# Kernel optimization log

Hardware: AMD Instinct MI355X
Metric: run time of the kernel (lower is better)

The kernel has to match this reference:

```python
import jax, jax.numpy as jnp
import numpy as np

WS, OWS, HEADS, DH = 8, 12, 4, 16
INNER = HEADS * DH
DIM = 64
RATIO = 0.5
REL = 12  # rel_size = WS + (OWS - WS)


def _conv1x1(x, W, b):
    return jnp.einsum('oc,bchw->bohw', W, x) + b[None, :, None, None]


def _lrelu(x):
    return jnp.where(x >= 0, x, 0.1 * x)


def _rel_to_abs(x):
    # x: [b, l, 2r-1] -> [b, l, r]
    b, l, m = x.shape
    r = (m + 1) // 2
    x = jnp.pad(x, ((0, 0), (0, 0), (0, 1))).reshape(b, l * (m + 1))
    x = jnp.pad(x, ((0, 0), (0, m - l))).reshape(b, l + 1, m)
    return x[:, :l, -r:]


def _relative_logits_1d(q, rel_k):
    # q: [b, h, w, d], rel_k: [2r-1, d] -> [b, h, r, w, r]
    b, h, w, _ = q.shape
    r = (rel_k.shape[0] + 1) // 2
    logits = jnp.einsum('bxyd,rd->bxyr', q, rel_k)
    logits = _rel_to_abs(logits.reshape(b * h, w, 2 * r - 1)).reshape(b, h, w, r)
    return jnp.broadcast_to(logits[:, :, None], (b, h, r, w, r))


def _rel_pos_emb(q, rel_h, rel_w):
    # q: [b, WS*WS, DH] -> [b, WS*WS, REL*REL]
    b = q.shape[0]
    q = q.reshape(b, WS, WS, DH)
    lw = _relative_logits_1d(q, rel_w)                        # [b, x, i, y, j]
    lw = lw.transpose(0, 1, 3, 2, 4).reshape(b, WS * WS, REL * REL)   # (x y),(i j)
    lh = _relative_logits_1d(q.transpose(0, 2, 1, 3), rel_h)  # [b, y, i, x, j]
    lh = lh.transpose(0, 3, 1, 4, 2).reshape(b, WS * WS, REL * REL)   # (x y),(j i)
    return lw + lh


def _windows(t, B, Hw, Ww):
    # 'b c (h p1) (w p2) -> b (h w) (p1 p2 c)'
    return t.reshape(B, INNER, Hw, WS, Ww, WS).transpose(0, 2, 4, 3, 5, 1).reshape(B, Hw * Ww, WS * WS * INNER)


def _forward(x, condition_global, Wq, bq, Wk, bk, Wv, bv, Wout, bout,
             rel_h, rel_w, pin_W, pin_b, ln_w, ln_b, sa_W, sa_b,
             m1_W, m1_b, m2_W, m2_b):
    B, C, H, W = x.shape
    Hw, Ww = H // WS, W // WS
    Nw = Hw * Ww
    keep = int(Nw * RATIO)  # deterministic num_keep_node (expected r=0.5)
    scale = DH ** -0.5

    qs = _conv1x1(x, Wq, bq)
    ks = _conv1x1(x, Wk, bk)
    vs = _conv1x1(x, Wv, bv)

    # condition_wind: stacked ij meshgrid of linspace(-1,1,WS), tiled over windows
    lin = jnp.linspace(-1.0, 1.0, WS)
    gy, gx = jnp.meshgrid(lin, lin, indexing='ij')
    wind = jnp.tile(jnp.stack([gy, gx]).astype(x.dtype)[None], (B, 1, Hw, Ww))
    cond = jnp.concatenate([vs, condition_global, wind], axis=1)  # [B, INNER+4, H, W]

    # PredictorLG
    h1 = _conv1x1(cond, pin_W, pin_b)
    u = h1.mean(1, keepdims=True)
    s = ((h1 - u) ** 2).mean(1, keepdims=True)
    h1 = ln_w[None, :, None, None] * (h1 - u) / jnp.sqrt(s + 1e-6) + ln_b[None, :, None, None]
    h1 = _lrelu(h1)
    sa = jax.lax.conv_general_dilated(h1, sa_W, (1, 1), ((1, 1), (1, 1)),
                                      dimension_numbers=('NCHW', 'OIHW', 'NCHW'))
    sa = jax.nn.sigmoid(sa + sa_b[None, :, None, None])          # [B,1,H,W]

    xm = h1.mean(1)                                               # [B,H,W]
    xm = xm.reshape(B, Hw, WS, Ww, WS).transpose(0, 1, 3, 2, 4).reshape(B, Nw, WS * WS)
    z = _lrelu(xm @ m1_W.T + m1_b)
    pred = jax.nn.softmax(z @ m2_W.T + m2_b, axis=-1)
    score = pred[:, :, 0]
    idx = jnp.argsort(-score, axis=1)
    idx1, idx2 = idx[:, :keep], idx[:, keep:]
    bar = jnp.arange(B)[:, None]

    v_easy = vs * sa

    qw = _windows(qs, B, Hw, Ww)                                  # [B, Nw, 64*INNER]

    pad = (OWS - WS) // 2
    def unfold(t):
        p = jax.lax.conv_general_dilated_patches(t, (OWS, OWS), (WS, WS),
                                                 [(pad, pad), (pad, pad)])
        # [B, INNER*OWS*OWS, Hw, Ww], channel-major (c, kh, kw) like torch unfold
        p = p.reshape(B, INNER, OWS * OWS, Nw)
        return p.transpose(0, 3, 2, 1).reshape(B, Nw, OWS * OWS * INNER)  # (j c)
    kw, vw = unfold(ks), unfold(vs)

    qk, kk, vk = qw[bar, idx1], kw[bar, idx1], vw[bar, idx1]       # gather hard windows

    def heads(t, ntok):
        return t.reshape(B * keep, ntok, HEADS, DH).transpose(0, 2, 1, 3).reshape(B * keep * HEADS, ntok, DH)
    qh = heads(qk, WS * WS) * scale
    kh = heads(kk, OWS * OWS)
    vh = heads(vk, OWS * OWS)

    attn = jnp.einsum('bqc,bkc->bqk', qh, kh) + _rel_pos_emb(qh, rel_h, rel_w)
    attn = jax.nn.softmax(attn, axis=-1)
    vo = jnp.einsum('bqk,bkc->bqc', attn, vh)                      # [B*keep*HEADS, 64, DH]

    # '(b j head) (p1 p2) c -> b j (p1 p2 head c)'
    v1 = vo.reshape(B, keep, HEADS, WS * WS, DH).transpose(0, 1, 3, 2, 4).reshape(B, keep, WS * WS * INNER)
    v2 = _windows(v_easy, B, Hw, Ww)[bar, idx2]

    out = jnp.zeros((B, Nw, WS * WS * INNER), x.dtype)
    out = out.at[bar, idx1].set(v1).at[bar, idx2].set(v2)          # batch_index_fill
    # 'b (h w) (dh dw c) -> b c (h dh) (w dw)'
    out = out.reshape(B, Hw, Ww, WS, WS, INNER).transpose(0, 5, 1, 3, 2, 4).reshape(B, INNER, H, W)
    return _conv1x1(out, Wout, bout)


def setup_inputs() -> dict:
    key = jax.random.key(0)
    k = jax.random.split(key, 16)
    B, H, W = 2, 256, 256
    cdim = INNER + 4
    rel_scale = DH ** -0.5

    def p(kk, shape, s=0.05):
        return jax.random.normal(kk, shape, jnp.float32) * s

    return {
        'x': jax.random.normal(k[0], (B, DIM, H, W), jnp.float32),
        'condition_global': jax.random.normal(k[1], (B, 2, H, W), jnp.float32),
        'Wq': p(k[2], (INNER, DIM)), 'bq': jnp.zeros((INNER,), jnp.float32),
        'Wk': p(k[3], (INNER, DIM)), 'bk': jnp.zeros((INNER,), jnp.float32),
        'Wv': p(k[4], (INNER, DIM)), 'bv': jnp.zeros((INNER,), jnp.float32),
        'Wout': p(k[5], (DIM, INNER)), 'bout': jnp.zeros((DIM,), jnp.float32),
        'rel_h': jax.random.normal(k[6], (2 * REL - 1, DH), jnp.float32) * rel_scale,
        'rel_w': jax.random.normal(k[7], (2 * REL - 1, DH), jnp.float32) * rel_scale,
        'pin_W': p(k[8], (cdim // 4, cdim)), 'pin_b': jnp.zeros((cdim // 4,), jnp.float32),
        'ln_w': jnp.ones((cdim // 4,), jnp.float32), 'ln_b': jnp.zeros((cdim // 4,), jnp.float32),
        'sa_W': p(k[9], (1, cdim // 4, 3, 3)), 'sa_b': jnp.zeros((1,), jnp.float32),
        'm1_W': p(k[10], (WS, WS * WS)), 'm1_b': jnp.zeros((WS,), jnp.float32),
        'm2_W': p(k[11], (2, WS)), 'm2_b': jnp.zeros((2,), jnp.float32),
    }


def reference(x, condition_global, Wq, bq, Wk, bk, Wv, bv, Wout, bout,
              rel_h, rel_w, pin_W, pin_b, ln_w, ln_b, sa_W, sa_b,
              m1_W, m1_b, m2_W, m2_b):
    return _forward(x, condition_global, Wq, bq, Wk, bk, Wv, bv, Wout, bout,
                    rel_h, rel_w, pin_W, pin_b, ln_w, ln_b, sa_W, sa_b,
                    m1_W, m1_b, m2_W, m2_b)
```

## Files before the change

kernel.cpp:

```cpp
#include <hip/hip_runtime.h>
#include <math.h>

#define NPIX   65536
#define NPIXT  131072
#define NW     1024
#define KEEP   512


__device__ __forceinline__ float bcast(float v, int l) {
    return __int_as_float(__builtin_amdgcn_readlane(__float_as_int(v), l));
}

__global__ __launch_bounds__(256) void k_qkv(
    const float* __restrict__ x,
    const float* __restrict__ Wq, const float* __restrict__ bq,
    const float* __restrict__ Wk, const float* __restrict__ bk,
    const float* __restrict__ Wv, const float* __restrict__ bv,
    float* __restrict__ qs, float* __restrict__ ks, float* __restrict__ vs)
{
    __shared__ float Wt[64][68];
    const int tid  = threadIdx.x;
    const int lane = tid & 63;
    const int og   = __builtin_amdgcn_readfirstlane(tid >> 6);
    const int tile = blockIdx.x;
    const int b    = tile >> 9;
    const int p0   = (tile & 511) << 7;
    const int p    = p0 + 2 * lane;
    const int gp   = (b << 16) + p;
    const int wo   = og * 16;

    const float* Ws[3]   = {Wq, Wk, Wv};
    const float* bias[3] = {bq, bk, bv};
    float* outs[3] = {qs + (size_t)gp * 64, ks + (size_t)gp * 64, vs + (size_t)gp * 64};
    const float* xg = x + ((size_t)b * 64) * NPIX + p;

    #pragma unroll
    for (int m = 0; m < 3; ++m) {
        __syncthreads();
        const float* Wm = Ws[m];
        #pragma unroll
        for (int it = 0; it < 4; ++it) {
            const int i  = it * 256 + tid;
            const int o  = i >> 4;
            const int c4 = i & 15;
            const float4 w = *(const float4*)(Wm + o * 64 + c4 * 4);
            Wt[c4 * 4 + 0][o] = w.x;
            Wt[c4 * 4 + 1][o] = w.y;
            Wt[c4 * 4 + 2][o] = w.z;
            Wt[c4 * 4 + 3][o] = w.w;
        }
        __syncthreads();

        float acc0[16], acc1[16];
        #pragma unroll
        for (int j = 0; j < 16; ++j) { acc0[j] = 0.f; acc1[j] = 0.f; }

        #pragma unroll 4
        for (int c = 0; c < 64; ++c) {
            const float2 xv = *(const float2*)(xg + (size_t)c * NPIX);
            const float4 w0 = *(const float4*)&Wt[c][wo + 0];
            const float4 w1 = *(const float4*)&Wt[c][wo + 4];
            const float4 w2 = *(const float4*)&Wt[c][wo + 8];
            const float4 w3 = *(const float4*)&Wt[c][wo + 12];
            acc0[0]  += w0.x * xv.x; acc1[0]  += w0.x * xv.y;
            acc0[1]  += w0.y * xv.x; acc1[1]  += w0.y * xv.y;
            acc0[2]  += w0.z * xv.x; acc1[2]  += w0.z * xv.y;
            acc0[3]  += w0.w * xv.x; acc1[3]  += w0.w * xv.y;
            acc0[4]  += w1.x * xv.x; acc1[4]  += w1.x * xv.y;
            acc0[5]  += w1.y * xv.x; acc1[5]  += w1.y * xv.y;
            acc0[6]  += w1.z * xv.x; acc1[6]  += w1.z * xv.y;
            acc0[7]  += w1.w * xv.x; acc1[7]  += w1.w * xv.y;
            acc0[8]  += w2.x * xv.x; acc1[8]  += w2.x * xv.y;
            acc0[9]  += w2.y * xv.x; acc1[9]  += w2.y * xv.y;
            acc0[10] += w2.z * xv.x; acc1[10] += w2.z * xv.y;
            acc0[11] += w2.w * xv.x; acc1[11] += w2.w * xv.y;
            acc0[12] += w3.x * xv.x; acc1[12] += w3.x * xv.y;
            acc0[13] += w3.y * xv.x; acc1[13] += w3.y * xv.y;
            acc0[14] += w3.z * xv.x; acc1[14] += w3.z * xv.y;
            acc0[15] += w3.w * xv.x; acc1[15] += w3.w * xv.y;
        }

        const float* bb = bias[m];
        float* o0 = outs[m];
        #pragma unroll
        for (int j4 = 0; j4 < 4; ++j4) {
            float4 v0, v1;
            v0.x = acc0[j4*4+0] + bb[wo + j4*4+0]; v1.x = acc1[j4*4+0] + bb[wo + j4*4+0];
            v0.y = acc0[j4*4+1] + bb[wo + j4*4+1]; v1.y = acc1[j4*4+1] + bb[wo + j4*4+1];
            v0.z = acc0[j4*4+2] + bb[wo + j4*4+2]; v1.z = acc1[j4*4+2] + bb[wo + j4*4+2];
            v0.w = acc0[j4*4+3] + bb[wo + j4*4+3]; v1.w = acc1[j4*4+3] + bb[wo + j4*4+3];
            *(float4*)(o0 + wo + j4*4)      = v0;
            *(float4*)(o0 + 64 + wo + j4*4) = v1;
        }
    }
}

__global__ __launch_bounds__(256) void k_cond(
    const float* __restrict__ vs, const float* __restrict__ cg,
    const float* __restrict__ pinW, const float* __restrict__ pinb,
    const float* __restrict__ lnw, const float* __restrict__ lnb,
    float* __restrict__ h1, float* __restrict__ xm)
{
    const int gp = blockIdx.x * 256 + threadIdx.x;
    const int b  = gp >> 16;
    const int p  = gp & 65535;
    const int h  = p >> 8;
    const int w  = p & 255;

    float acc[17];
    #pragma unroll
    for (int oc = 0; oc < 17; ++oc) acc[oc] = pinb[oc];

    const float* vp = vs + (size_t)gp * 64;
    #pragma unroll 8
    for (int c4 = 0; c4 < 16; ++c4) {
        const float4 v4 = *(const float4*)(vp + c4 * 4);
        const float vv[4] = {v4.x, v4.y, v4.z, v4.w};
        #pragma unroll
        for (int k = 0; k < 4; ++k) {
            const int c = c4 * 4 + k;
            #pragma unroll
            for (int oc = 0; oc < 17; ++oc)
                acc[oc] += pinW[oc * 68 + c] * vv[k];
        }
    }
    const float c64 = cg[(b * 2 + 0) * NPIX + p];
    const float c65 = cg[(b * 2 + 1) * NPIX + p];
    const float c66 = -1.f + 2.f * (float)(h & 7) / 7.f;
    const float c67 = -1.f + 2.f * (float)(w & 7) / 7.f;
    #pragma unroll
    for (int oc = 0; oc < 17; ++oc)
        acc[oc] += pinW[oc * 68 + 64] * c64 + pinW[oc * 68 + 65] * c65 +
                   pinW[oc * 68 + 66] * c66 + pinW[oc * 68 + 67] * c67;

    float u = 0.f;
    #pragma unroll
    for (int oc = 0; oc < 17; ++oc) u += acc[oc];
    u *= (1.f / 17.f);
    float s = 0.f;
    #pragma unroll
    for (int oc = 0; oc < 17; ++oc) { const float d = acc[oc] - u; s += d * d; }
    s *= (1.f / 17.f);
    const float rstd = rsqrtf(s + 1e-6f);

    float xsum = 0.f;
    #pragma unroll
    for (int oc = 0; oc < 17; ++oc) {
        float hv = lnw[oc] * (acc[oc] - u) * rstd + lnb[oc];
        hv = (hv >= 0.f) ? hv : 0.1f * hv;
        h1[(b * 17 + oc) * NPIX + p] = hv;
        xsum += hv;
    }
    const int win = (h >> 3) * 32 + (w >> 3);
    const int idx = ((h & 7) << 3) | (w & 7);
    xm[(b << 16) + win * 64 + idx] = xsum * (1.f / 17.f);
}

__global__ __launch_bounds__(256) void k_sa(
    const float* __restrict__ h1, const float* __restrict__ saW,
    const float* __restrict__ sab, float* __restrict__ sa)
{
    __shared__ float S[17 * 3 * 256];
    const int tid = threadIdx.x;
    const int b   = blockIdx.x >> 8;
    const int row = blockIdx.x & 255;

    for (int i = tid; i < 3264; i += 256) {
        const int ch  = i / 192;
        const int rem = i - ch * 192;
        const int dr  = rem >> 6;
        const int c4  = rem & 63;
        const int rr  = row + dr - 1;
        float4 v = {0.f, 0.f, 0.f, 0.f};
        if ((unsigned)rr < 256u)
            v = *(const float4*)(h1 + ((size_t)(b * 17 + ch)) * NPIX + rr * 256 + c4 * 4);
        *(float4*)&S[(ch * 3 + dr) * 256 + c4 * 4] = v;
    }
    __syncthreads();

    const int w = tid;
    float acc = sab[0];
    #pragma unroll 1
    for (int ch = 0; ch < 17; ++ch) {
        #pragma unroll
        for (int dr = 0; dr < 3; ++dr) {
            const float* Sp = &S[(ch * 3 + dr) * 256];
            const float m  = Sp[w];
            const float l  = (w > 0)   ? Sp[w - 1] : 0.f;
            const float r_ = (w < 255) ? Sp[w + 1] : 0.f;
            const float* Wp = saW + (ch * 3 + dr) * 3;
            acc += Wp[0] * l + Wp[1] * m + Wp[2] * r_;
        }
    }
    sa[b * NPIX + row * 256 + w] = 1.f / (1.f + __expf(-acc));
}

__global__ __launch_bounds__(1024) void k_score_select(
    const float* __restrict__ xm,
    const float* __restrict__ m1W, const float* __restrict__ m1b,
    const float* __restrict__ m2W, const float* __restrict__ m2b,
    int* __restrict__ flag, int* __restrict__ kept)
{
    __shared__ float sc[NW];
    const int b = blockIdx.x;
    const int t = threadIdx.x;

    float z[8];
    #pragma unroll
    for (int jj = 0; jj < 8; ++jj) z[jj] = m1b[jj];

    const float* xw = xm + (b << 16) + t * 64;
    #pragma unroll 4
    for (int t4 = 0; t4 < 16; ++t4) {
        const float4 v4 = *(const float4*)(xw + t4 * 4);
        const float vv[4] = {v4.x, v4.y, v4.z, v4.w};
        #pragma unroll
        for (int k = 0; k < 4; ++k) {
            const int tt = t4 * 4 + k;
            #pragma unroll
            for (int jj = 0; jj < 8; ++jj)
                z[jj] += m1W[jj * 64 + tt] * vv[k];
        }
    }
    #pragma unroll
    for (int jj = 0; jj < 8; ++jj) z[jj] = (z[jj] >= 0.f) ? z[jj] : 0.1f * z[jj];

    float l0 = m2b[0], l1 = m2b[1];
    #pragma unroll
    for (int jj = 0; jj < 8; ++jj) { l0 += m2W[jj] * z[jj]; l1 += m2W[8 + jj] * z[jj]; }
    const float mx = fmaxf(l0, l1);
    const float e0 = expf(l0 - mx), e1 = expf(l1 - mx);
    sc[t] = e0 / (e0 + e1);
    __syncthreads();

    const float s = sc[t];
    int cnt = 0;
    for (int jq = 0; jq < NW; jq += 4) {
        const float4 s4 = *(const float4*)&sc[jq];
        cnt += (s4.x > s) || (s4.x == s && (jq + 0) < t);
        cnt += (s4.y > s) || (s4.y == s && (jq + 1) < t);
        cnt += (s4.z > s) || (s4.z == s && (jq + 2) < t);
        cnt += (s4.w > s) || (s4.w == s && (jq + 3) < t);
    }
    flag[b * NW + t] = (cnt < KEEP) ? 1 : 0;
    if (cnt < KEEP) kept[b * KEEP + cnt] = t;
}

__global__ __launch_bounds__(256) void k_attn(
    const float* __restrict__ qs, const float* __restrict__ ks,
    const float* __restrict__ vs, const int* __restrict__ kept,
    const float* __restrict__ relh, const float* __restrict__ relw,
    float* __restrict__ amix)
{
    __shared__ float SK[144 * 64];
    __shared__ float CW[12 * 256];
    const int b    = blockIdx.y;
    const int win  = kept[b * KEEP + blockIdx.x];
    const int wy = win >> 5, wx = win & 31;
    const int tid  = threadIdx.x;
    const int head = __builtin_amdgcn_readfirstlane(tid >> 6);
    const int lane = tid & 63;
    const int choff = head * 16;
    const size_t bbase = (size_t)b * NPIX;
    const int px0 = (wy * 8) * 256 + wx * 8;
    const int qrow = lane >> 3, qcol = lane & 7;
    const int sub = lane >> 4, d_ = lane & 15;
    const int wy8 = wy * 8 - 2, wx8 = wx * 8 - 2;

    #pragma unroll
    for (int it = 0; it < 9; ++it) {
        const int i   = it * 256 + tid;
        const int pxl = i >> 4;
        const int c4  = i & 15;
        const int rl  = pxl / 12;
        const int col = pxl - rl * 12;
        const int ry  = wy8 + rl;
        const int cx  = wx8 + col;
        float4 kv = {0.f, 0.f, 0.f, 0.f};
        if ((unsigned)ry < 256u && (unsigned)cx < 256u)
            kv = *(const float4*)(ks + (bbase + (size_t)(ry * 256 + cx)) * 64 + c4 * 4);
        *(float4*)&SK[pxl * 64 + c4 * 4] = kv;
    }

    float q[16];
    {
        const float* qp = qs + (bbase + px0 + qrow * 256 + qcol) * 64 + choff;
        #pragma unroll
        for (int j4 = 0; j4 < 4; ++j4) {
            const float4 v = *(const float4*)(qp + j4 * 4);
            q[j4 * 4 + 0] = v.x * 0.25f; q[j4 * 4 + 1] = v.y * 0.25f;
            q[j4 * 4 + 2] = v.z * 0.25f; q[j4 * 4 + 3] = v.w * 0.25f;
        }
    }

    #pragma unroll
    for (int k = 0; k < 12; ++k) {
        const float* rw = relw + (k - qcol + 11) * 16;
        float sw = 0.f;
        #pragma unroll
        for (int j4 = 0; j4 < 4; ++j4) {
            const float4 w4 = *(const float4*)(rw + j4 * 4);
            sw += q[j4*4+0]*w4.x + q[j4*4+1]*w4.y + q[j4*4+2]*w4.z + q[j4*4+3]*w4.w;
        }
        CW[k * 256 + tid] = sw;
    }

    const int laneoff = choff + d_;

    float sum = 0.f;
    float vo[16];
    #pragma unroll
    for (int d = 0; d < 16; ++d) vo[d] = 0.f;

    __syncthreads();

    #pragma unroll 1
    for (int r = 0; r < 12; ++r) {
        const int ry = wy8 + r;
        const bool rowok = (unsigned)ry < 256u;

        float vg0 = 0.f, vg1 = 0.f, vg2 = 0.f;
        if (rowok) {
            const size_t rowa = bbase + (size_t)(ry * 256);
            const int cx0 = wx8 + sub, cx1 = cx0 + 4, cx2 = cx0 + 8;
            if ((unsigned)cx0 < 256u) vg0 = vs[(rowa + cx0) * 64 + laneoff];
            if ((unsigned)cx1 < 256u) vg1 = vs[(rowa + cx1) * 64 + laneoff];
            if ((unsigned)cx2 < 256u) vg2 = vs[(rowa + cx2) * 64 + laneoff];
        }

        const float* rh = relh + (r - qrow + 11) * 16;
        float srow = 0.f;
        #pragma unroll
        for (int j4 = 0; j4 < 4; ++j4) {
            const float4 h4 = *(const float4*)(rh + j4 * 4);
            srow += q[j4*4+0]*h4.x + q[j4*4+1]*h4.y + q[j4*4+2]*h4.z + q[j4*4+3]*h4.w;
        }

        #pragma unroll
        for (int gi = 0; gi < 3; ++gi) {
            const float vg = (gi == 0) ? vg0 : (gi == 1) ? vg1 : vg2;
            #pragma unroll
            for (int kk = 0; kk < 4; ++kk) {
                const int col = 4 * gi + kk;
                const float* kb = &SK[(r * 12 + col) * 64 + choff];
                const float4 k0 = *(const float4*)(kb + 0);
                const float4 k1 = *(const float4*)(kb + 4);
                const float4 k2 = *(const float4*)(kb + 8);
                const float4 k3 = *(const float4*)(kb + 12);
                float s = srow + CW[col * 256 + tid];
                s += k0.x*q[0];  s += k0.y*q[1];  s += k0.z*q[2];  s += k0.w*q[3];
                s += k1.x*q[4];  s += k1.y*q[5];  s += k1.z*q[6];  s += k1.w*q[7];
                s += k2.x*q[8];  s += k2.y*q[9];  s += k2.z*q[10]; s += k2.w*q[11];
                s += k3.x*q[12]; s += k3.y*q[13]; s += k3.z*q[14]; s += k3.w*q[15];
                const float e = __expf(s);
                sum += e;
                vo[0]  += e * bcast(vg, kk * 16 + 0);
                vo[1]  += e * bcast(vg, kk * 16 + 1);
                vo[2]  += e * bcast(vg, kk * 16 + 2);
                vo[3]  += e * bcast(vg, kk * 16 + 3);
                vo[4]  += e * bcast(vg, kk * 16 + 4);
                vo[5]  += e * bcast(vg, kk * 16 + 5);
                vo[6]  += e * bcast(vg, kk * 16 + 6);
                vo[7]  += e * bcast(vg, kk * 16 + 7);
                vo[8]  += e * bcast(vg, kk * 16 + 8);
                vo[9]  += e * bcast(vg, kk * 16 + 9);
                vo[10] += e * bcast(vg, kk * 16 + 10);
                vo[11] += e * bcast(vg, kk * 16 + 11);
                vo[12] += e * bcast(vg, kk * 16 + 12);
                vo[13] += e * bcast(vg, kk * 16 + 13);
                vo[14] += e * bcast(vg, kk * 16 + 14);
                vo[15] += e * bcast(vg, kk * 16 + 15);
            }
        }
    }

    const float inv = 1.f / sum;
    float* op = amix + (bbase + px0 + qrow * 256 + qcol) * 64 + choff;
    #pragma unroll
    for (int j4 = 0; j4 < 4; ++j4) {
        float4 v;
        v.x = vo[j4*4+0] * inv; v.y = vo[j4*4+1] * inv;
        v.z = vo[j4*4+2] * inv; v.w = vo[j4*4+3] * inv;
        *(float4*)(op + j4 * 4) = v;
    }
}

__global__ __launch_bounds__(256) void k_out_f(
    const float* __restrict__ amix, const float* __restrict__ vs,
    const float* __restrict__ sa, const int* __restrict__ flag,
    const float* __restrict__ W, const float* __restrict__ bias,
    float* __restrict__ out)
{
    __shared__ float xs[64][130];
    __shared__ float Wt[64][68];
    __shared__ float smult[128];
    __shared__ int   sflag[128];
    const int tid  = threadIdx.x;
    const int lane = tid & 63;
    const int og   = __builtin_amdgcn_readfirstlane(tid >> 6);
    const int tile = blockIdx.x;
    const int b    = tile >> 9;
    const int p0   = (tile & 511) << 7;
    const int wo   = og * 16;

    #pragma unroll
    for (int it = 0; it < 4; ++it) {
        const int i  = it * 256 + tid;
        const int o  = i >> 4;
        const int c4 = i & 15;
        const float4 w = *(const float4*)(W + o * 64 + c4 * 4);
        Wt[c4 * 4 + 0][o] = w.x;
        Wt[c4 * 4 + 1][o] = w.y;
        Wt[c4 * 4 + 2][o] = w.z;
        Wt[c4 * 4 + 3][o] = w.w;
    }

    if (tid < 128) {
        const int p   = p0 + tid;
        const int h   = p >> 8, w_ = p & 255;
        const int win = (h >> 3) * 32 + (w_ >> 3);
        const int fl  = flag[b * NW + win];
        sflag[tid] = fl;
        smult[tid] = fl ? 1.f : sa[(b << 16) + p];
    }
    __syncthreads();

    #pragma unroll
    for (int it = 0; it < 8; ++it) {
        const int i   = it * 256 + tid;
        const int pxl = i >> 4;
        const int c4  = i & 15;
        const int gpl = (b << 16) + p0 + pxl;
        const float* src = (sflag[pxl] ? amix : vs) + (size_t)gpl * 64;
        const float m = smult[pxl];
        const float4 v = *(const float4*)(src + c4 * 4);
        xs[c4 * 4 + 0][pxl] = v.x * m;
        xs[c4 * 4 + 1][pxl] = v.y * m;
        xs[c4 * 4 + 2][pxl] = v.z * m;
        xs[c4 * 4 + 3][pxl] = v.w * m;
    }
    __syncthreads();

    float acc0[16], acc1[16];
    #pragma unroll
    for (int j = 0; j < 16; ++j) { acc0[j] = 0.f; acc1[j] = 0.f; }

    #pragma unroll 4
    for (int c = 0; c < 64; ++c) {
        const float2 xv = *(const float2*)&xs[c][2 * lane];
        const float4 w0 = *(const float4*)&Wt[c][wo + 0];
        const float4 w1 = *(const float4*)&Wt[c][wo + 4];
        const float4 w2 = *(const float4*)&Wt[c][wo + 8];
        const float4 w3 = *(const float4*)&Wt[c][wo + 12];
        acc0[0]  += w0.x * xv.x; acc1[0]  += w0.x * xv.y;
        acc0[1]  += w0.y * xv.x; acc1[1]  += w0.y * xv.y;
        acc0[2]  += w0.z * xv.x; acc1[2]  += w0.z * xv.y;
        acc0[3]  += w0.w * xv.x; acc1[3]  += w0.w * xv.y;
        acc0[4]  += w1.x * xv.x; acc1[4]  += w1.x * xv.y;
        acc0[5]  += w1.y * xv.x; acc1[5]  += w1.y * xv.y;
        acc0[6]  += w1.z * xv.x; acc1[6]  += w1.z * xv.y;
        acc0[7]  += w1.w * xv.x; acc1[7]  += w1.w * xv.y;
        acc0[8]  += w2.x * xv.x; acc1[8]  += w2.x * xv.y;
        acc0[9]  += w2.y * xv.x; acc1[9]  += w2.y * xv.y;
        acc0[10] += w2.z * xv.x; acc1[10] += w2.z * xv.y;
        acc0[11] += w2.w * xv.x; acc1[11] += w2.w * xv.y;
        acc0[12] += w3.x * xv.x; acc1[12] += w3.x * xv.y;
        acc0[13] += w3.y * xv.x; acc1[13] += w3.y * xv.y;
        acc0[14] += w3.z * xv.x; acc1[14] += w3.z * xv.y;
        acc0[15] += w3.w * xv.x; acc1[15] += w3.w * xv.y;
    }

    const int p    = p0 + 2 * lane;
    const int base = (b << 6) * NPIX + p;
    #pragma unroll
    for (int j = 0; j < 16; ++j) {
        const float bj = bias[wo + j];
        out[base +     (wo + j) * NPIX] = acc0[j] + bj;
        out[base + 1 + (wo + j) * NPIX] = acc1[j] + bj;
    }
}

extern "C" void kernel_launch(void* const* d_in, const int* in_sizes, int n_in,
                              void* d_out, int out_size, void* d_ws, size_t ws_size,
                              hipStream_t stream)
{
    const float* x    = (const float*)d_in[0];
    const float* cg   = (const float*)d_in[1];
    const float* Wq   = (const float*)d_in[2];
    const float* bq   = (const float*)d_in[3];
    const float* Wk   = (const float*)d_in[4];
    const float* bk   = (const float*)d_in[5];
    const float* Wv   = (const float*)d_in[6];
    const float* bv   = (const float*)d_in[7];
    const float* Wout = (const float*)d_in[8];
    const float* bout = (const float*)d_in[9];
    const float* relh = (const float*)d_in[10];
    const float* relw = (const float*)d_in[11];
    const float* pinW = (const float*)d_in[12];
    const float* pinb = (const float*)d_in[13];
    const float* lnw  = (const float*)d_in[14];
    const float* lnb  = (const float*)d_in[15];
    const float* saW  = (const float*)d_in[16];
    const float* sab  = (const float*)d_in[17];
    const float* m1W  = (const float*)d_in[18];
    const float* m1b  = (const float*)d_in[19];
    const float* m2W  = (const float*)d_in[20];
    const float* m2b  = (const float*)d_in[21];
    float* out = (float*)d_out;

    float* ws    = (float*)d_ws;
    float* qs    = ws;
    float* ks    = qs + 8388608;
    float* vs    = ks + 8388608;
    float* h1    = vs + 8388608;
    float* xm    = h1 + 17 * NPIXT;
    float* sa    = xm + NPIXT;
    int*   flag  = (int*)(sa + NPIXT);
    int*   kept  = flag + 2048;

    k_qkv         <<<1024, 256, 0, stream>>>(x, Wq, bq, Wk, bk, Wv, bv, qs, ks, vs);
    k_cond        <<<NPIXT / 256, 256, 0, stream>>>(vs, cg, pinW, pinb, lnw, lnb, h1, xm);
    k_sa          <<<512, 256, 0, stream>>>(h1, saW, sab, sa);
    k_score_select<<<2, 1024, 0, stream>>>(xm, m1W, m1b, m2W, m2b, flag, kept);
    k_attn        <<<dim3(KEEP, 2), 256, 0, stream>>>(qs, ks, vs, kept, relh, relw, qs);
    k_out_f       <<<1024, 256, 0, stream>>>(qs, vs, sa, flag, Wout, bout, out);
}
```

Baseline: 359.5 us.

## Restructure QKV projection tiling and halve attention K shared-memory footprint

```diff
diff --git a/kernel.cpp b/kernel.cpp
--- a/kernel.cpp
+++ b/kernel.cpp
@@ -18,14 +18,14 @@
     const float* __restrict__ Wv, const float* __restrict__ bv,
     float* __restrict__ qs, float* __restrict__ ks, float* __restrict__ vs)
 {
-    __shared__ float Wt[64][68];
+    __shared__ float Wt[3][64][68];
     const int tid  = threadIdx.x;
     const int lane = tid & 63;
     const int og   = __builtin_amdgcn_readfirstlane(tid >> 6);
     const int tile = blockIdx.x;
-    const int b    = tile >> 9;
-    const int p0   = (tile & 511) << 7;
-    const int p    = p0 + 2 * lane;
+    const int b    = tile >> 8;
+    const int p0   = (tile & 255) << 8;
+    const int p    = p0 + 4 * lane;
     const int gp   = (b << 16) + p;
     const int wo   = og * 16;
 
@@ -35,62 +35,58 @@
     const float* xg = x + ((size_t)b * 64) * NPIX + p;
 
     #pragma unroll
+    for (int it = 0; it < 12; ++it) {
+        const int i   = it * 256 + tid;
+        const int m   = i >> 10;
+        const int rem = i & 1023;
+        const int o   = rem >> 4;
+        const int c4  = rem & 15;
+        const float4 w = *(const float4*)(Ws[m] + o * 64 + c4 * 4);
+        Wt[m][c4 * 4 + 0][o] = w.x;
+        Wt[m][c4 * 4 + 1][o] = w.y;
+        Wt[m][c4 * 4 + 2][o] = w.z;
+        Wt[m][c4 * 4 + 3][o] = w.w;
+    }
+    __syncthreads();
+
+    #pragma unroll
     for (int m = 0; m < 3; ++m) {
-        __syncthreads();
-        const float* Wm = Ws[m];
         #pragma unroll
-        for (int it = 0; it < 4; ++it) {
-            const int i  = it * 256 + tid;
-            const int o  = i >> 4;
-            const int c4 = i & 15;
-            const float4 w = *(const float4*)(Wm + o * 64 + c4 * 4);
-            Wt[c4 * 4 + 0][o] = w.x;
-            Wt[c4 * 4 + 1][o] = w.y;
-            Wt[c4 * 4 + 2][o] = w.z;
-            Wt[c4 * 4 + 3][o] = w.w;
-        }
-        __syncthreads();
-
-        float acc0[16], acc1[16];
-        #pragma unroll
-        for (int j = 0; j < 16; ++j) { acc0[j] = 0.f; acc1[j] = 0.f; }
-
-        #pragma unroll 4
-        for (int c = 0; c < 64; ++c) {
-            const float2 xv = *(const float2*)(xg + (size_t)c * NPIX);
-            const float4 w0 = *(const float4*)&Wt[c][wo + 0];
-            const float4 w1 = *(const float4*)&Wt[c][wo + 4];
-            const float4 w2 = *(const float4*)&Wt[c][wo + 8];
-            const float4 w3 = *(const float4*)&Wt[c][wo + 12];
-            acc0[0]  += w0.x * xv.x; acc1[0]  += w0.x * xv.y;
-            acc0[1]  += w0.y * xv.x; acc1[1]  += w0.y * xv.y;
-            acc0[2]  += w0.z * xv.x; acc1[2]  += w0.z * xv.y;
-            acc0[3]  += w0.w * xv.x; acc1[3]  += w0.w * xv.y;
-            acc0[4]  += w1.x * xv.x; acc1[4]  += w1.x * xv.y;
-            acc0[5]  += w1.y * xv.x; acc1[5]  += w1.y * xv.y;
-            acc0[6]  += w1.z * xv.x; acc1[6]  += w1.z * xv.y;
-            acc0[7]  += w1.w * xv.x; acc1[7]  += w1.w * xv.y;
-            acc0[8]  += w2.x * xv.x; acc1[8]  += w2.x * xv.y;
-            acc0[9]  += w2.y * xv.x; acc1[9]  += w2.y * xv.y;
-            acc0[10] += w2.z * xv.x; acc1[10] += w2.z * xv.y;
-            acc0[11] += w2.w * xv.x; acc1[11] += w2.w * xv.y;
-            acc0[12] += w3.x * xv.x; acc1[12] += w3.x * xv.y;
-            acc0[13] += w3.y * xv.x; acc1[13] += w3.y * xv.y;
-            acc0[14] += w3.z * xv.x; acc1[14] += w3.z * xv.y;
-            acc0[15] += w3.w * xv.x; acc1[15] += w3.w * xv.y;
-        }
-
-        const float* bb = bias[m];
-        float* o0 = outs[m];
-        #pragma unroll
-        for (int j4 = 0; j4 < 4; ++j4) {
-            float4 v0, v1;
-            v0.x = acc0[j4*4+0] + bb[wo + j4*4+0]; v1.x = acc1[j4*4+0] + bb[wo + j4*4+0];
-            v0.y = acc0[j4*4+1] + bb[wo + j4*4+1]; v1.y = acc1[j4*4+1] + bb[wo + j4*4+1];
-            v0.z = acc0[j4*4+2] + bb[wo + j4*4+2]; v1.z = acc1[j4*4+2] + bb[wo + j4*4+2];
-            v0.w = acc0[j4*4+3] + bb[wo + j4*4+3]; v1.w = acc1[j4*4+3] + bb[wo + j4*4+3];
-            *(float4*)(o0 + wo + j4*4)      = v0;
-            *(float4*)(o0 + 64 + wo + j4*4) = v1;
+        for (int hh = 0; hh < 2; ++hh) {
+            const int o0 = wo + 8 * hh;
+            float acc[4][8];
+            #pragma unroll
+            for (int k = 0; k < 4; ++k)
+                #pragma unroll
+                for (int j = 0; j < 8; ++j) acc[k][j] = 0.f;
+
+            #pragma unroll 4
+            for (int c = 0; c < 64; ++c) {
+                const float4 xv = *(const float4*)(xg + (size_t)c * NPIX);
+                const float4 w0 = *(const float4*)&Wt[m][c][o0 + 0];
+                const float4 w1 = *(const float4*)&Wt[m][c][o0 + 4];
+                const float xv4[4] = {xv.x, xv.y, xv.z, xv.w};
+                const float wv[8]  = {w0.x, w0.y, w0.z, w0.w,
+                                      w1.x, w1.y, w1.z, w1.w};
+                #pragma unroll
+                for (int k = 0; k < 4; ++k)
+                    #pragma unroll
+                    for (int j = 0; j < 8; ++j)
+                        acc[k][j] += wv[j] * xv4[k];
+            }
+
+            const float* bb = bias[m];
+            float* op = outs[m];
+            #pragma unroll
+            for (int k = 0; k < 4; ++k) {
+                float4 v0, v1;
+                v0.x = acc[k][0] + bb[o0 + 0]; v0.y = acc[k][1] + bb[o0 + 1];
+                v0.z = acc[k][2] + bb[o0 + 2]; v0.w = acc[k][3] + bb[o0 + 3];
+                v1.x = acc[k][4] + bb[o0 + 4]; v1.y = acc[k][5] + bb[o0 + 5];
+                v1.z = acc[k][6] + bb[o0 + 6]; v1.w = acc[k][7] + bb[o0 + 7];
+                *(float4*)(op + k * 64 + o0 + 0) = v0;
+                *(float4*)(op + k * 64 + o0 + 4) = v1;
+            }
         }
     }
 }
@@ -252,7 +248,7 @@
     const float* __restrict__ relh, const float* __restrict__ relw,
     float* __restrict__ amix)
 {
-    __shared__ float SK[144 * 64];
+    __shared__ float SK[72 * 64];
     __shared__ float CW[12 * 256];
     const int b    = blockIdx.y;
     const int win  = kept[b * KEEP + blockIdx.x];
@@ -267,21 +263,6 @@
     const int sub = lane >> 4, d_ = lane & 15;
     const int wy8 = wy * 8 - 2, wx8 = wx * 8 - 2;
 
-    #pragma unroll
-    for (int it = 0; it < 9; ++it) {
-        const int i   = it * 256 + tid;
-        const int pxl = i >> 4;
-        const int c4  = i & 15;
-        const int rl  = pxl / 12;
-        const int col = pxl - rl * 12;
-        const int ry  = wy8 + rl;
-        const int cx  = wx8 + col;
-        float4 kv = {0.f, 0.f, 0.f, 0.f};
-        if ((unsigned)ry < 256u && (unsigned)cx < 256u)
-            kv = *(const float4*)(ks + (bbase + (size_t)(ry * 256 + cx)) * 64 + c4 * 4);
-        *(float4*)&SK[pxl * 64 + c4 * 4] = kv;
-    }
-
     float q[16];
     {
         const float* qp = qs + (bbase + px0 + qrow * 256 + qcol) * 64 + choff;
@@ -312,64 +293,81 @@
     #pragma unroll
     for (int d = 0; d < 16; ++d) vo[d] = 0.f;
 
-    __syncthreads();
-
     #pragma unroll 1
-    for (int r = 0; r < 12; ++r) {
-        const int ry = wy8 + r;
-        const bool rowok = (unsigned)ry < 256u;
-
-        float vg0 = 0.f, vg1 = 0.f, vg2 = 0.f;
-        if (rowok) {
-            const size_t rowa = bbase + (size_t)(ry * 256);
-            const int cx0 = wx8 + sub, cx1 = cx0 + 4, cx2 = cx0 + 8;
-            if ((unsigned)cx0 < 256u) vg0 = vs[(rowa + cx0) * 64 + laneoff];
-            if ((unsigned)cx1 < 256u) vg1 = vs[(rowa + cx1) * 64 + laneoff];
-            if ((unsigned)cx2 < 256u) vg2 = vs[(rowa + cx2) * 64 + laneoff];
-        }
-
-        const float* rh = relh + (r - qrow + 11) * 16;
-        float srow = 0.f;
-        #pragma unroll
-        for (int j4 = 0; j4 < 4; ++j4) {
-            const float4 h4 = *(const float4*)(rh + j4 * 4);
-            srow += q[j4*4+0]*h4.x + q[j4*4+1]*h4.y + q[j4*4+2]*h4.z + q[j4*4+3]*h4.w;
-        }
-
-        #pragma unroll
-        for (int gi = 0; gi < 3; ++gi) {
-            const float vg = (gi == 0) ? vg0 : (gi == 1) ? vg1 : vg2;
+    for (int ch = 0; ch < 2; ++ch) {
+        __syncthreads();
+        for (int i = tid; i < 1152; i += 256) {
+            const int pxl = i >> 4;
+            const int c4  = i & 15;
+            const int rl  = pxl / 12;
+            const int col = pxl - rl * 12;
+            const int ry  = wy8 + 6 * ch + rl;
+            const int cx  = wx8 + col;
+            float4 kv = {0.f, 0.f, 0.f, 0.f};
+            if ((unsigned)ry < 256u && (unsigned)cx < 256u)
+                kv = *(const float4*)(ks + (bbase + (size_t)(ry * 256 + cx)) * 64 + c4 * 4);
+            *(float4*)&SK[pxl * 64 + c4 * 4] = kv;
+        }
+        __syncthreads();
+
+        #pragma unroll 1
+        for (int rl = 0; rl < 6; ++rl) {
+            const int r  = 6 * ch + rl;
+            const int ry = wy8 + r;
+            const bool rowok = (unsigned)ry < 256u;
+
+            float vg0 = 0.f, vg1 = 0.f, vg2 = 0.f;
+            if (rowok) {
+                const size_t rowa = bbase + (size_t)(ry * 256);
+                const int cx0 = wx8 + sub, cx1 = cx0 + 4, cx2 = cx0 + 8;
+                if ((unsigned)cx0 < 256u) vg0 = vs[(rowa + cx0) * 64 + laneoff];
+                if ((unsigned)cx1 < 256u) vg1 = vs[(rowa + cx1) * 64 + laneoff];
+                if ((unsigned)cx2 < 256u) vg2 = vs[(rowa + cx2) * 64 + laneoff];
+            }
+
+            const float* rh = relh + (r - qrow + 11) * 16;
+            float srow = 0.f;
             #pragma unroll
-            for (int kk = 0; kk < 4; ++kk) {
-                const int col = 4 * gi + kk;
-                const float* kb = &SK[(r * 12 + col) * 64 + choff];
-                const float4 k0 = *(const float4*)(kb + 0);
-                const float4 k1 = *(const float4*)(kb + 4);
-                const float4 k2 = *(const float4*)(kb + 8);
-                const float4 k3 = *(const float4*)(kb + 12);
-                float s = srow + CW[col * 256 + tid];
-                s += k0.x*q[0];  s += k0.y*q[1];  s += k0.z*q[2];  s += k0.w*q[3];
-                s += k1.x*q[4];  s += k1.y*q[5];  s += k1.z*q[6];  s += k1.w*q[7];
-                s += k2.x*q[8];  s += k2.y*q[9];  s += k2.z*q[10]; s += k2.w*q[11];
-                s += k3.x*q[12]; s += k3.y*q[13]; s += k3.z*q[14]; s += k3.w*q[15];
-                const float e = __expf(s);
-                sum += e;
-                vo[0]  += e * bcast(vg, kk * 16 + 0);
-                vo[1]  += e * bcast(vg, kk * 16 + 1);
-                vo[2]  += e * bcast(vg, kk * 16 + 2);
-                vo[3]  += e * bcast(vg, kk * 16 + 3);
-                vo[4]  += e * bcast(vg, kk * 16 + 4);
-                vo[5]  += e * bcast(vg, kk * 16 + 5);
-                vo[6]  += e * bcast(vg, kk * 16 + 6);
-                vo[7]  += e * bcast(vg, kk * 16 + 7);
-                vo[8]  += e * bcast(vg, kk * 16 + 8);
-                vo[9]  += e * bcast(vg, kk * 16 + 9);
-                vo[10] += e * bcast(vg, kk * 16 + 10);
-                vo[11] += e * bcast(vg, kk * 16 + 11);
-                vo[12] += e * bcast(vg, kk * 16 + 12);
-                vo[13] += e * bcast(vg, kk * 16 + 13);
-                vo[14] += e * bcast(vg, kk * 16 + 14);
-                vo[15] += e * bcast(vg, kk * 16 + 15);
+            for (int j4 = 0; j4 < 4; ++j4) {
+                const float4 h4 = *(const float4*)(rh + j4 * 4);
+                srow += q[j4*4+0]*h4.x + q[j4*4+1]*h4.y + q[j4*4+2]*h4.z + q[j4*4+3]*h4.w;
+            }
+
+            #pragma unroll
+            for (int gi = 0; gi < 3; ++gi) {
+                const float vg = (gi == 0) ? vg0 : (gi == 1) ? vg1 : vg2;
+                #pragma unroll
+                for (int kk = 0; kk < 4; ++kk) {
+                    const int col = 4 * gi + kk;
+                    const float* kb = &SK[(rl * 12 + col) * 64 + choff];
+                    const float4 k0 = *(const float4*)(kb + 0);
+                    const float4 k1 = *(const float4*)(kb + 4);
+                    const float4 k2 = *(const float4*)(kb + 8);
+                    const float4 k3 = *(const float4*)(kb + 12);
+                    float s = srow + CW[col * 256 + tid];
+                    s += k0.x*q[0];  s += k0.y*q[1];  s += k0.z*q[2];  s += k0.w*q[3];
+                    s += k1.x*q[4];  s += k1.y*q[5];  s += k1.z*q[6];  s += k1.w*q[7];
+                    s += k2.x*q[8];  s += k2.y*q[9];  s += k2.z*q[10]; s += k2.w*q[11];
+                    s += k3.x*q[12]; s += k3.y*q[13]; s += k3.z*q[14]; s += k3.w*q[15];
+                    const float e = __expf(s);
+                    sum += e;
+                    vo[0]  += e * bcast(vg, kk * 16 + 0);
+                    vo[1]  += e * bcast(vg, kk * 16 + 1);
+                    vo[2]  += e * bcast(vg, kk * 16 + 2);
+                    vo[3]  += e * bcast(vg, kk * 16 + 3);
+                    vo[4]  += e * bcast(vg, kk * 16 + 4);
+                    vo[5]  += e * bcast(vg, kk * 16 + 5);
+                    vo[6]  += e * bcast(vg, kk * 16 + 6);
+                    vo[7]  += e * bcast(vg, kk * 16 + 7);
+                    vo[8]  += e * bcast(vg, kk * 16 + 8);
+                    vo[9]  += e * bcast(vg, kk * 16 + 9);
+                    vo[10] += e * bcast(vg, kk * 16 + 10);
+                    vo[11] += e * bcast(vg, kk * 16 + 11);
+                    vo[12] += e * bcast(vg, kk * 16 + 12);
+                    vo[13] += e * bcast(vg, kk * 16 + 13);
+                    vo[14] += e * bcast(vg, kk * 16 + 14);
+                    vo[15] += e * bcast(vg, kk * 16 + 15);
+                }
             }
         }
     }
@@ -518,7 +516,7 @@
     int*   flag  = (int*)(sa + NPIXT);
     int*   kept  = flag + 2048;
 
-    k_qkv         <<<1024, 256, 0, stream>>>(x, Wq, bq, Wk, bk, Wv, bv, qs, ks, vs);
+    k_qkv         <<<512, 256, 0, stream>>>(x, Wq, bq, Wk, bk, Wv, bv, qs, ks, vs);
     k_cond        <<<NPIXT / 256, 256, 0, stream>>>(vs, cg, pinW, pinb, lnw, lnb, h1, xm);
     k_sa          <<<512, 256, 0, stream>>>(h1, saW, sab, sa);
     k_score_select<<<2, 1024, 0, stream>>>(xm, m1W, m1b, m2W, m2b, flag, kept);
```

After: 380.2 us. +5.7%, slower.
